# Kernel tuning notes

Measured on AMD Instinct MI355X. Metric: run time of the kernel, lower is better.

Reference implementation:

```python
import jax, jax.numpy as jnp
import numpy as np

PATCH_SIZE = 50        # hardcoded in forward (overrides __init__ args)
NUM_PATCHES_OUT = 50   # size of the weighted_x buffer
TOPK = 4


def setup_inputs() -> dict:
    key = jax.random.key(0)
    k1, k2 = jax.random.split(key)
    x = jax.random.normal(k1, (1024, 12, 2500), dtype=jnp.float32)
    # self.weights = sigmoid(sample from N(0,1)) -> a scalar in (0,1)
    weights = jax.nn.sigmoid(jax.random.normal(k2, (), dtype=jnp.float32))
    return {"x": x, "weights": weights}


def reference(x, weights):
    B, N, L = x.shape
    # power spectrum |FFT(x)|^2 along time axis
    power = jnp.abs(jnp.fft.fft(x, axis=2)) ** 2            # [B,N,L] f32
    _, idx = jax.lax.top_k(power, TOPK)                      # [B,N,K] descending
    # only lead 0 and topk positions {0, 2} are used by the original code
    idx2 = idx[:, 0, ::2]                                    # [B,2] int32
    # np.fft.fftfreq(L)[i] = i/L for i <= (L-1)//2 else (i-L)/L
    k_signed = jnp.where(idx2 <= (L - 1) // 2, idx2, idx2 - L)
    valid = k_signed != 0                                    # freq == 0 -> skip
    # ideal_peak_interval = int(|1/freq|) = L // |k| (exact integer math)
    period = L // jnp.maximum(jnp.abs(k_signed), 1)          # [B,2] >= 2
    P = L // PATCH_SIZE                                      # effective num_patches
    starts = jnp.arange(P, dtype=jnp.int32) * PATCH_SIZE     # [P]
    # patch [start, start+PATCH_SIZE) contains a peak (multiple of period)
    # iff the first multiple >= start is < start + PATCH_SIZE
    p = period[..., None]                                    # [B,2,1]
    first_mult = ((starts[None, None, :] + p - 1) // p) * p  # [B,2,P]
    hit = (first_mult < starts[None, None, :] + PATCH_SIZE) & valid[..., None]
    counts = hit.sum(axis=1)                                 # [B,P] in {0,1,2}
    # the b/n loops add `weights` N times per (b, patch, freq-slot) hit
    weighted = (N * weights) * counts.astype(jnp.float32)    # [B,P]
    out = jnp.zeros((B, NUM_PATCHES_OUT), jnp.float32).at[:, :P].set(weighted)
    # original detaches via a numpy round-trip -> no gradient flows
    return jax.lax.stop_gradient(out)
```

## Files before the change

kernel.cpp:

```cpp
#include <hip/hip_runtime.h>

typedef _Float16 f16;
typedef _Float16 f16x2 __attribute__((ext_vector_type(2)));
typedef _Float16 f16x4 __attribute__((ext_vector_type(4)));
typedef _Float16 f16x8 __attribute__((ext_vector_type(8)));
typedef float f32x4 __attribute__((ext_vector_type(4)));

#define L_N 2500
#define B_N 1024
#define ROWSTRIDE 30000
#define NPATCH 50
#define PATCH 50
#define KP 2560
#define NB 2560
#define ZSPLIT 4
#define KS_PER_Z 20

#define TWOPI_F 6.28318530717958647692f
#define RAD_PER_PH (6.283185307179586476925286766559 / 2500.0)

#define OFF_XH 0
#define SZ_XH (B_N * KP * 2)
#define OFF_W  (OFF_XH + SZ_XH)
#define SZ_W   (NB * KP * 2)
#define OFF_P  (OFF_W + SZ_W)
#define SZ_P   (ZSPLIT * B_N * NB * 4)

#define PB_X    B_N
#define PB_W    1280
#define PB_TOT  (PB_X + PB_W)

#define GLOAD16(gp, lp) __builtin_amdgcn_global_load_lds( \
    (const __attribute__((address_space(1))) unsigned int*)(gp), \
    (__attribute__((address_space(3))) unsigned int*)(lp), 16, 0, 0)

__global__ __launch_bounds__(256)
void prep(const float* __restrict__ x, f16* __restrict__ Xh, f16* __restrict__ W) {
    const int b = blockIdx.x, tid = threadIdx.x;
    if (b < PB_X) {
        const int row = b;
#pragma unroll
        for (int i = 0; i < 3; ++i) {
            int slot = tid + 256 * i;
            if (slot < 640) {
                float4 v = make_float4(0.f, 0.f, 0.f, 0.f);
                if (slot < 625)
                    v = *reinterpret_cast<const float4*>(x + (size_t)row * ROWSTRIDE + slot * 4);
                f16x4 h = { (f16)v.x, (f16)v.y, (f16)v.z, (f16)v.w };
                *reinterpret_cast<f16x4*>(Xh + (size_t)row * KP + slot * 4) = h;
            }
        }
    } else {
        const int bin = b - PB_X;
#pragma unroll
        for (int i = 0; i < 5; ++i) {
            int t2 = tid + 256 * i;
            int t = 2 * t2;
            float c0 = 0.f, s0 = 0.f, c1 = 0.f, s1 = 0.f;
            if (t < L_N) {
                int ph = (bin * t) % L_N;
                float th = (float)ph * (TWOPI_F / (float)L_N);
                __sincosf(th, &s0, &c0);
            }
            if (t + 1 < L_N) {
                int ph = (bin * (t + 1)) % L_N;
                float th = (float)ph * (TWOPI_F / (float)L_N);
                __sincosf(th, &s1, &c1);
            }
            f16x2 cc = { (f16)c0, (f16)c1 };
            f16x2 ss = { (f16)s0, (f16)s1 };
            *reinterpret_cast<f16x2*>(&W[(size_t)(2 * bin) * KP + t])     = cc;
            *reinterpret_cast<f16x2*>(&W[(size_t)(2 * bin + 1) * KP + t]) = ss;
        }
    }
}

__global__ __launch_bounds__(256)
void gemm_f16(const f16* __restrict__ A, const f16* __restrict__ W, float* __restrict__ P) {
    __shared__ f16 As[2][128 * 32];
    __shared__ f16 Bs[2][128 * 32];
    const int tid = threadIdx.x;
    const int wv = tid >> 6, lane = tid & 63;
    const int bm = blockIdx.x, bn = blockIdx.y;
    const int ks0 = blockIdx.z * KS_PER_Z;
    const int wr = wv >> 1, wc = wv & 1;
    const int lrow = lane & 15, lseg = lane >> 4;

    f32x4 acc[4][4];
#pragma unroll
    for (int m = 0; m < 4; ++m)
#pragma unroll
        for (int n = 0; n < 4; ++n) acc[m][n] = (f32x4){0.f, 0.f, 0.f, 0.f};

    const int c0 = wv * 128 + lane, c1 = c0 + 64;
    const int R0 = c0 >> 2, S0 = (c0 & 3) ^ ((R0 >> 1) & 3);
    const int R1 = c1 >> 2, S1 = (c1 & 3) ^ ((R1 >> 1) & 3);
    const f16* ga0 = A + (size_t)(bm * 128 + R0) * KP + S0 * 8;
    const f16* ga1 = A + (size_t)(bm * 128 + R1) * KP + S1 * 8;
    const f16* gb0 = W + (size_t)(bn * 128 + R0) * KP + S0 * 8;
    const f16* gb1 = W + (size_t)(bn * 128 + R1) * KP + S1 * 8;

    int aoff[4], boff[4];
#pragma unroll
    for (int m = 0; m < 4; ++m) {
        int ra = wr * 64 + m * 16 + lrow;
        aoff[m] = ra * 32 + ((lseg ^ ((ra >> 1) & 3)) * 8);
        int rb = wc * 64 + m * 16 + lrow;
        boff[m] = rb * 32 + ((lseg ^ ((rb >> 1) & 3)) * 8);
    }

    {
        const int kof = ks0 * 32;
        GLOAD16(ga0 + kof, &As[0][c0 * 8]);
        GLOAD16(ga1 + kof, &As[0][c1 * 8]);
        GLOAD16(gb0 + kof, &Bs[0][c0 * 8]);
        GLOAD16(gb1 + kof, &Bs[0][c1 * 8]);
    }
    __syncthreads();

    int cur = 0;
    for (int t = 0; t < KS_PER_Z; ++t) {
        const int nxt = cur ^ 1;
        if (t + 1 < KS_PER_Z) {
            const int kof = (ks0 + t + 1) * 32;
            GLOAD16(ga0 + kof, &As[nxt][c0 * 8]);
            GLOAD16(ga1 + kof, &As[nxt][c1 * 8]);
            GLOAD16(gb0 + kof, &Bs[nxt][c0 * 8]);
            GLOAD16(gb1 + kof, &Bs[nxt][c1 * 8]);
        }
        f16x8 af[4], bf[4];
#pragma unroll
        for (int m = 0; m < 4; ++m) af[m] = *(const f16x8*)&As[cur][aoff[m]];
#pragma unroll
        for (int n = 0; n < 4; ++n) bf[n] = *(const f16x8*)&Bs[cur][boff[n]];
#pragma unroll
        for (int m = 0; m < 4; ++m)
#pragma unroll
            for (int n = 0; n < 4; ++n)
                acc[m][n] = __builtin_amdgcn_mfma_f32_16x16x32_f16(af[m], bf[n], acc[m][n], 0, 0, 0);
        __syncthreads();
        cur = nxt;
    }

    float* Pz = P + (size_t)blockIdx.z * B_N * NB;
    const int orow0 = bm * 128 + wr * 64 + (lane >> 4) * 4;
    const int ocol0 = bn * 128 + wc * 64 + (lane & 15);
#pragma unroll
    for (int m = 0; m < 4; ++m)
#pragma unroll
        for (int n = 0; n < 4; ++n)
#pragma unroll
            for (int j = 0; j < 4; ++j)
                Pz[(size_t)(orow0 + m * 16 + j) * NB + ocol0 + n * 16] = acc[m][n][j];
}

__global__ __launch_bounds__(512)
void fused_sel(const float* __restrict__ x, const float* __restrict__ P,
               const float* __restrict__ wp, float* __restrict__ out) {
    __shared__ float xrow[KP];
    __shared__ unsigned long long keybuf[64];
    __shared__ int bins8s[8];
    __shared__ unsigned long long rk[8];
    const int row = blockIdx.x, tid = threadIdx.x;
    const int wv = tid >> 6, lane = tid & 63;

    if (tid < 60) xrow[2500 + tid] = 0.f;
#pragma unroll
    for (int i = 0; i < 2; ++i) {
        int slot = tid + 512 * i;
        if (slot < 625)
            *reinterpret_cast<float4*>(&xrow[slot * 4]) =
                *reinterpret_cast<const float4*>(x + (size_t)row * ROWSTRIDE + slot * 4);
    }

    unsigned long long k3[3];
#pragma unroll
    for (int c = 0; c < 3; ++c) {
        int bin = tid + 512 * c;
        unsigned long long key = 0ULL;
        if (bin <= 1250) {
            float re = 0.f, im = 0.f;
#pragma unroll
            for (int s2 = 0; s2 < ZSPLIT; ++s2) {
                float2 ri = *reinterpret_cast<const float2*>(
                    &P[((size_t)s2 * B_N + row) * NB + 2 * bin]);
                re += ri.x; im += ri.y;
            }
            float p = re * re + im * im;
            key = ((unsigned long long)__float_as_uint(p) << 32) | (unsigned)(L_N - bin);
        }
        k3[c] = key;
    }
#pragma unroll
    for (int r = 0; r < 8; ++r) {
        unsigned long long m = k3[0];
        m = (k3[1] > m) ? k3[1] : m;
        m = (k3[2] > m) ? k3[2] : m;
#pragma unroll
        for (int off = 32; off > 0; off >>= 1) {
            unsigned long long o = __shfl_xor(m, off, 64);
            m = (o > m) ? o : m;
        }
        if (k3[0] == m) k3[0] = 0ULL;
        if (k3[1] == m) k3[1] = 0ULL;
        if (k3[2] == m) k3[2] = 0ULL;
        if (lane == 0) keybuf[wv * 8 + r] = m;
    }
    __syncthreads();
    if (wv == 0) {
        unsigned long long cur = keybuf[lane];
#pragma unroll
        for (int r = 0; r < 8; ++r) {
            unsigned long long m = cur;
#pragma unroll
            for (int off = 32; off > 0; off >>= 1) {
                unsigned long long o = __shfl_xor(m, off, 64);
                m = (o > m) ? o : m;
            }
            if (cur == m) cur = 0ULL;
            if (lane == 0) bins8s[r] = L_N - (int)(unsigned)(m & 0xffffffffULL);
        }
    }
    __syncthreads();

    const int k = bins8s[wv];
    double c, s, cd, sd;
    {
        int ph0 = (k * lane) % L_N;
        int phd = (k * 64) % L_N;
        sincos((double)ph0 * RAD_PER_PH, &s, &c);
        sincos((double)phd * RAD_PER_PH, &sd, &cd);
    }
    double re = 0.0, im = 0.0;
#pragma unroll 4
    for (int i = 0; i < 40; ++i) {
        double xv = (double)xrow[lane + 64 * i];
        re += xv * c;
        im += xv * s;
        double cn = c * cd - s * sd;
        double sn = s * cd + c * sd;
        c = cn; s = sn;
    }
#pragma unroll
    for (int off = 32; off > 0; off >>= 1) {
        re += __shfl_xor(re, off, 64);
        im += __shfl_xor(im, off, 64);
    }
    if (lane == 0) {
        double p = re * re + im * im;
        unsigned long long pb = (unsigned long long)__double_as_longlong(p);
        rk[wv] = (pb & ~2047ULL) | (unsigned long long)(1250 - k);
    }
    __syncthreads();

    if (tid < NPATCH) {
        unsigned long long q[8];
#pragma unroll
        for (int r = 0; r < 8; ++r) q[r] = rk[r];
        unsigned long long m1 = q[0];
#pragma unroll
        for (int r = 1; r < 8; ++r) m1 = (q[r] > m1) ? q[r] : m1;
#pragma unroll
        for (int r = 0; r < 8; ++r) if (q[r] == m1) q[r] = 0;
        unsigned long long m2 = q[0];
#pragma unroll
        for (int r = 1; r < 8; ++r) m2 = (q[r] > m2) ? q[r] : m2;
#pragma unroll
        for (int r = 0; r < 8; ++r) if (q[r] == m2) q[r] = 0;
        unsigned long long m3 = q[0];
#pragma unroll
        for (int r = 1; r < 8; ++r) m3 = (q[r] > m3) ? q[r] : m3;

        int kA = 1250 - (int)(m1 & 2047ULL);
        int kB = 1250 - (int)(m2 & 2047ULL);
        int kC = 1250 - (int)(m3 & 2047ULL);
        int multA = (kA == 0 || kA == 1250) ? 1 : 2;
        int multB = (kB == 0 || kB == 1250) ? 1 : 2;
        int sel0 = kA;
        int sel1 = (multA == 2 || multB == 2) ? kB : kC;

        int start = tid * PATCH;
        int cnt = 0;
        if (sel0 != 0) {
            int p = L_N / sel0;
            int fm = ((start + p - 1) / p) * p;
            if (fm < start + PATCH) ++cnt;
        }
        if (sel1 != 0) {
            int p = L_N / sel1;
            int fm = ((start + p - 1) / p) * p;
            if (fm < start + PATCH) ++cnt;
        }
        out[(size_t)row * NPATCH + tid] = 12.0f * wp[0] * (float)cnt;
    }
}

extern "C" void kernel_launch(void* const* d_in, const int* in_sizes, int n_in,
                              void* d_out, int out_size, void* d_ws, size_t ws_size,
                              hipStream_t stream) {
    const float* x = (const float*)d_in[0];
    const float* w = (const float*)d_in[1];
    float* out = (float*)d_out;
    char* ws = (char*)d_ws;

    f16* Xh = (f16*)(ws + OFF_XH);
    f16* W  = (f16*)(ws + OFF_W);
    float* P = (float*)(ws + OFF_P);

    prep<<<PB_TOT, 256, 0, stream>>>(x, Xh, W);
    gemm_f16<<<dim3(8, 20, ZSPLIT), 256, 0, stream>>>(Xh, W, P);
    fused_sel<<<B_N, 512, 0, stream>>>(x, P, w, out);
}
```

Before: 208.1 us.

## Drop split-K, shrink GEMM tiles, and fuse power computation into GEMM epilogue

Removes the 4-way split-K partial-sum buffer. Each block now covers a 64x64 tile over the full K range, and the epilogue squares the real and imaginary accumulators and combines adjacent columns with a lane shuffle. The result is a compact power array that is half the width and one quarter the count of partial buffers. This cuts the large fp32 partial-sum write and re-read traffic and the reduction in the selection kernel. In exchange, the smaller tiles lower MFMA reuse per LDS load and the longer serial K loop per block may lower compute efficiency.

```diff
diff --git a/kernel.cpp b/kernel.cpp
--- a/kernel.cpp
+++ b/kernel.cpp
@@ -13,8 +13,8 @@
 #define PATCH 50
 #define KP 2560
 #define NB 2560
-#define ZSPLIT 4
-#define KS_PER_Z 20
+#define NPOW 1280
+#define KS_TOT 80
 
 #define TWOPI_F 6.28318530717958647692f
 #define RAD_PER_PH (6.283185307179586476925286766559 / 2500.0)
@@ -24,7 +24,7 @@
 #define OFF_W  (OFF_XH + SZ_XH)
 #define SZ_W   (NB * KP * 2)
 #define OFF_P  (OFF_W + SZ_W)
-#define SZ_P   (ZSPLIT * B_N * NB * 4)
+#define SZ_P   (B_N * NPOW * 4)
 
 #define PB_X    B_N
 #define PB_W    1280
@@ -76,86 +76,84 @@
 }
 
 __global__ __launch_bounds__(256)
-void gemm_f16(const f16* __restrict__ A, const f16* __restrict__ W, float* __restrict__ P) {
-    __shared__ f16 As[2][128 * 32];
-    __shared__ f16 Bs[2][128 * 32];
+void gemm_f16(const f16* __restrict__ A, const f16* __restrict__ W, float* __restrict__ Pow) {
+    __shared__ f16 As[2][64 * 32];
+    __shared__ f16 Bs[2][64 * 32];
     const int tid = threadIdx.x;
     const int wv = tid >> 6, lane = tid & 63;
     const int bm = blockIdx.x, bn = blockIdx.y;
-    const int ks0 = blockIdx.z * KS_PER_Z;
     const int wr = wv >> 1, wc = wv & 1;
     const int lrow = lane & 15, lseg = lane >> 4;
 
-    f32x4 acc[4][4];
-#pragma unroll
-    for (int m = 0; m < 4; ++m)
-#pragma unroll
-        for (int n = 0; n < 4; ++n) acc[m][n] = (f32x4){0.f, 0.f, 0.f, 0.f};
-
-    const int c0 = wv * 128 + lane, c1 = c0 + 64;
-    const int R0 = c0 >> 2, S0 = (c0 & 3) ^ ((R0 >> 1) & 3);
-    const int R1 = c1 >> 2, S1 = (c1 & 3) ^ ((R1 >> 1) & 3);
-    const f16* ga0 = A + (size_t)(bm * 128 + R0) * KP + S0 * 8;
-    const f16* ga1 = A + (size_t)(bm * 128 + R1) * KP + S1 * 8;
-    const f16* gb0 = W + (size_t)(bn * 128 + R0) * KP + S0 * 8;
-    const f16* gb1 = W + (size_t)(bn * 128 + R1) * KP + S1 * 8;
-
-    int aoff[4], boff[4];
-#pragma unroll
-    for (int m = 0; m < 4; ++m) {
-        int ra = wr * 64 + m * 16 + lrow;
+    f32x4 acc[2][2];
+#pragma unroll
+    for (int m = 0; m < 2; ++m)
+#pragma unroll
+        for (int n = 0; n < 2; ++n) acc[m][n] = (f32x4){0.f, 0.f, 0.f, 0.f};
+
+    const int R0 = tid >> 2, S0 = (tid & 3) ^ ((R0 >> 1) & 3);
+    const f16* ga0 = A + (size_t)(bm * 64 + R0) * KP + S0 * 8;
+    const f16* gb0 = W + (size_t)(bn * 64 + R0) * KP + S0 * 8;
+    const int ldst = tid * 8;
+
+    int aoff[2], boff[2];
+#pragma unroll
+    for (int m = 0; m < 2; ++m) {
+        int ra = wr * 32 + m * 16 + lrow;
         aoff[m] = ra * 32 + ((lseg ^ ((ra >> 1) & 3)) * 8);
-        int rb = wc * 64 + m * 16 + lrow;
+        int rb = wc * 32 + m * 16 + lrow;
         boff[m] = rb * 32 + ((lseg ^ ((rb >> 1) & 3)) * 8);
     }
 
-    {
-        const int kof = ks0 * 32;
-        GLOAD16(ga0 + kof, &As[0][c0 * 8]);
-        GLOAD16(ga1 + kof, &As[0][c1 * 8]);
-        GLOAD16(gb0 + kof, &Bs[0][c0 * 8]);
-        GLOAD16(gb1 + kof, &Bs[0][c1 * 8]);
-    }
+    GLOAD16(ga0, &As[0][ldst]);
+    GLOAD16(gb0, &Bs[0][ldst]);
     __syncthreads();
 
     int cur = 0;
-    for (int t = 0; t < KS_PER_Z; ++t) {
+    for (int t = 0; t < KS_TOT; ++t) {
         const int nxt = cur ^ 1;
-        if (t + 1 < KS_PER_Z) {
-            const int kof = (ks0 + t + 1) * 32;
-            GLOAD16(ga0 + kof, &As[nxt][c0 * 8]);
-            GLOAD16(ga1 + kof, &As[nxt][c1 * 8]);
-            GLOAD16(gb0 + kof, &Bs[nxt][c0 * 8]);
-            GLOAD16(gb1 + kof, &Bs[nxt][c1 * 8]);
-        }
-        f16x8 af[4], bf[4];
-#pragma unroll
-        for (int m = 0; m < 4; ++m) af[m] = *(const f16x8*)&As[cur][aoff[m]];
-#pragma unroll
-        for (int n = 0; n < 4; ++n) bf[n] = *(const f16x8*)&Bs[cur][boff[n]];
-#pragma unroll
-        for (int m = 0; m < 4; ++m)
-#pragma unroll
-            for (int n = 0; n < 4; ++n)
+        if (t + 1 < KS_TOT) {
+            const int kof = (t + 1) * 32;
+            GLOAD16(ga0 + kof, &As[nxt][ldst]);
+            GLOAD16(gb0 + kof, &Bs[nxt][ldst]);
+        }
+        f16x8 af[2], bf[2];
+#pragma unroll
+        for (int m = 0; m < 2; ++m) af[m] = *(const f16x8*)&As[cur][aoff[m]];
+#pragma unroll
+        for (int n = 0; n < 2; ++n) bf[n] = *(const f16x8*)&Bs[cur][boff[n]];
+#pragma unroll
+        for (int m = 0; m < 2; ++m)
+#pragma unroll
+            for (int n = 0; n < 2; ++n)
                 acc[m][n] = __builtin_amdgcn_mfma_f32_16x16x32_f16(af[m], bf[n], acc[m][n], 0, 0, 0);
         __syncthreads();
         cur = nxt;
     }
 
-    float* Pz = P + (size_t)blockIdx.z * B_N * NB;
-    const int orow0 = bm * 128 + wr * 64 + (lane >> 4) * 4;
-    const int ocol0 = bn * 128 + wc * 64 + (lane & 15);
-#pragma unroll
-    for (int m = 0; m < 4; ++m)
-#pragma unroll
-        for (int n = 0; n < 4; ++n)
-#pragma unroll
-            for (int j = 0; j < 4; ++j)
-                Pz[(size_t)(orow0 + m * 16 + j) * NB + ocol0 + n * 16] = acc[m][n][j];
+    const int rbase = bm * 64 + wr * 32 + (lane >> 4) * 4;
+    const int cbase = bn * 64 + wc * 32 + (lane & 15);
+#pragma unroll
+    for (int m = 0; m < 2; ++m)
+#pragma unroll
+        for (int n = 0; n < 2; ++n) {
+            f32x4 p2;
+#pragma unroll
+            for (int j = 0; j < 4; ++j) p2[j] = acc[m][n][j] * acc[m][n][j];
+#pragma unroll
+            for (int j = 0; j < 4; ++j) {
+                float ps = p2[j] + __shfl_xor(p2[j], 1, 64);
+                if (!(lane & 1)) {
+                    int row = rbase + m * 16 + j;
+                    int col = cbase + n * 16;
+                    Pow[(size_t)row * NPOW + (col >> 1)] = ps;
+                }
+            }
+        }
 }
 
 __global__ __launch_bounds__(512)
-void fused_sel(const float* __restrict__ x, const float* __restrict__ P,
+void fused_sel(const float* __restrict__ x, const float* __restrict__ Pow,
                const float* __restrict__ wp, float* __restrict__ out) {
     __shared__ float xrow[KP];
     __shared__ unsigned long long keybuf[64];
@@ -179,14 +177,7 @@
         int bin = tid + 512 * c;
         unsigned long long key = 0ULL;
         if (bin <= 1250) {
-            float re = 0.f, im = 0.f;
-#pragma unroll
-            for (int s2 = 0; s2 < ZSPLIT; ++s2) {
-                float2 ri = *reinterpret_cast<const float2*>(
-                    &P[((size_t)s2 * B_N + row) * NB + 2 * bin]);
-                re += ri.x; im += ri.y;
-            }
-            float p = re * re + im * im;
+            float p = Pow[(size_t)row * NPOW + bin];
             key = ((unsigned long long)__float_as_uint(p) << 32) | (unsigned)(L_N - bin);
         }
         k3[c] = key;
@@ -305,9 +296,9 @@
 
     f16* Xh = (f16*)(ws + OFF_XH);
     f16* W  = (f16*)(ws + OFF_W);
-    float* P = (float*)(ws + OFF_P);
+    float* Pow = (float*)(ws + OFF_P);
 
     prep<<<PB_TOT, 256, 0, stream>>>(x, Xh, W);
-    gemm_f16<<<dim3(8, 20, ZSPLIT), 256, 0, stream>>>(Xh, W, P);
-    fused_sel<<<B_N, 512, 0, stream>>>(x, P, w, out);
+    gemm_f16<<<dim3(16, 40), 256, 0, stream>>>(Xh, W, Pow);
+    fused_sel<<<B_N, 512, 0, stream>>>(x, Pow, w, out);
 }
```

New measurement: 216.5 us. 4.0% more time.
